# Performance work log

Measured on AMD Instinct MI355X. Metric: run time of the kernel, lower is better.

The kernel has to match this reference:

```python
import jax, jax.numpy as jnp
import numpy as np

K = 16  # num neighbors


def setup_inputs() -> dict:
    key = jax.random.key(0)
    ks = jax.random.split(key, 10)
    B, N, d_in, d_out = 4, 8192, 64, 128
    h = d_out // 2
    return {
        "xyz": jax.random.normal(ks[0], (B, 3, N), jnp.float32),
        "feature": jax.random.normal(ks[1], (B, d_in, N), jnp.float32),
        "w1": jax.random.normal(ks[2], (h, 10), jnp.float32) * 0.1,
        "b1": jax.random.normal(ks[3], (h,), jnp.float32) * 0.1,
        "w2": jax.random.normal(ks[4], (h, h), jnp.float32) * 0.1,
        "b2": jax.random.normal(ks[5], (h,), jnp.float32) * 0.1,
        "w3": jax.random.normal(ks[6], (h, h), jnp.float32) * 0.1,
        "b3": jax.random.normal(ks[7], (h,), jnp.float32) * 0.1,
        "ws": jax.random.normal(ks[8], (d_out, d_in), jnp.float32) * 0.1,
        "bs": jax.random.normal(ks[9], (d_out,), jnp.float32) * 0.1,
    }


def reference(xyz, feature, w1, b1, w2, b2, w3, b3, ws, bs):
    # xyz: [B,3,N], feature: [B,d_in,N]
    xyz_t = jnp.transpose(xyz, (0, 2, 1))  # [B,N,3]
    sq = jnp.sum(xyz_t * xyz_t, axis=-1)  # [B,N]
    # squared pairwise distance [B,N,N]
    dist = sq[:, :, None] + sq[:, None, :] - 2.0 * jnp.einsum("bnc,bmc->bnm", xyz_t, xyz_t)
    _, idx = jax.lax.top_k(-dist, K)  # smallest-k -> [B,N,K]
    # gather neighbor coords: [B,N,K,3]
    knn_xyz = jax.vmap(lambda pts, ind: pts[ind])(xyz_t, idx)
    center = jnp.broadcast_to(xyz_t[:, :, None, :], knn_xyz.shape)  # [B,N,K,3]
    diff = knn_xyz - center
    dsq = jnp.sum(diff * diff, axis=-1, keepdims=True)  # [B,N,K,1]
    pos = jnp.concatenate([center, knn_xyz, diff, dsq], axis=-1)  # [B,N,K,10]
    # three 1x1 convs over channel dim (no activations, faithful to source)
    h = jnp.einsum("bnkc,oc->bnko", pos, w1) + b1
    h = jnp.einsum("bnkc,oc->bnko", h, w2) + b2
    h = jnp.einsum("bnkc,oc->bnko", h, w3) + b3
    fe = jnp.max(h, axis=2)  # max-pool over neighbors -> [B,N,d_out//2]
    fe = jnp.transpose(fe, (0, 2, 1))  # [B,d_out//2,N]
    shortcut = jnp.einsum("bcn,oc->bon", feature, ws) + bs[None, :, None]
    return jnp.concatenate([fe, fe], axis=1) + shortcut  # [B,d_out,N]
```

## Files before the change

### kernel.cpp

```cpp
#include <hip/hip_runtime.h>

#define B_ 4
#define N_ 8192
#define DIN 64
#define HDIM 64
#define DOUT 128
#define KNN 16
#define QPB 64
#define PART 8
#define NTHR (QPB * PART)
#define CHUNK (N_ / PART)
#define CAP 16
#define BLOCKS_PER_B (N_ / QPB)

__global__ __launch_bounds__(256) void k_prep(
    const float* __restrict__ xyz,
    const float* __restrict__ w1, const float* __restrict__ b1,
    const float* __restrict__ w2, const float* __restrict__ b2,
    const float* __restrict__ w3, const float* __restrict__ b3,
    float4* __restrict__ pk, float4* __restrict__ prm) {
  const int blk = blockIdx.x, t = threadIdx.x;
  const int b = blk >> 5;
  const int m = ((blk & 31) << 8) + t;
  const float* xb = xyz + (size_t)b * 3 * N_;
  float x = xb[m], y = xb[N_ + m], z = xb[2 * N_ + m];
  float sq = __fadd_rn(__fadd_rn(__fmul_rn(x, x), __fmul_rn(y, y)), __fmul_rn(z, z));
  pk[((size_t)b << 13) + m] = make_float4(x, y, z, sq);

  if (blk == 0) {
    __shared__ float M2[HDIM][10];
    __shared__ float bb[HDIM];
    const int o = t;
    if (o < HDIM) {
      float r[10];
#pragma unroll
      for (int c = 0; c < 10; c++) r[c] = 0.f;
      float s = b2[o];
      for (int l = 0; l < HDIM; l++) {
        float w = w2[o * HDIM + l];
#pragma unroll
        for (int c = 0; c < 10; c++) r[c] = fmaf(w, w1[l * 10 + c], r[c]);
        s = fmaf(w, b1[l], s);
      }
#pragma unroll
      for (int c = 0; c < 10; c++) M2[o][c] = r[c];
      bb[o] = s;
    }
    __syncthreads();
    if (o < HDIM) {
      float r3[10];
#pragma unroll
      for (int c = 0; c < 10; c++) r3[c] = 0.f;
      float bc = b3[o];
      for (int l = 0; l < HDIM; l++) {
        float w = w3[o * HDIM + l];
#pragma unroll
        for (int c = 0; c < 10; c++) r3[c] = fmaf(w, M2[l][c], r3[c]);
        bc = fmaf(w, bb[l], bc);
      }
      prm[o]      = make_float4(r3[0] - r3[6], r3[1] - r3[7], r3[2] - r3[8], bc);
      prm[64 + o] = make_float4(r3[3] + r3[6], r3[4] + r3[7], r3[5] + r3[8], r3[9]);
    }
  }
}

#define INSERT16(VARR, IARR, VMAX, DVAL, MIDX)                    \
  {                                                               \
    bool done = false;                                            \
    _Pragma("unroll") for (int _i = 0; _i < KNN; _i++) {          \
      bool hit = (!done) && (VARR[_i] == VMAX);                   \
      if (hit) { VARR[_i] = (DVAL); IARR[_i] = (MIDX); }          \
      done = done | hit;                                          \
    }                                                             \
    float _a = fmaxf(fmaxf(fmaxf(VARR[0], VARR[1]), fmaxf(VARR[2], VARR[3])),   \
                     fmaxf(fmaxf(VARR[4], VARR[5]), fmaxf(VARR[6], VARR[7])));  \
    float _b = fmaxf(fmaxf(fmaxf(VARR[8], VARR[9]), fmaxf(VARR[10], VARR[11])), \
                     fmaxf(fmaxf(VARR[12], VARR[13]), fmaxf(VARR[14], VARR[15])));\
    VMAX = fmaxf(_a, _b);                                         \
  }

#define MAX16(VARR, VMAX)                                         \
  {                                                               \
    float _a = fmaxf(fmaxf(fmaxf(VARR[0], VARR[1]), fmaxf(VARR[2], VARR[3])),   \
                     fmaxf(fmaxf(VARR[4], VARR[5]), fmaxf(VARR[6], VARR[7])));  \
    float _b = fmaxf(fmaxf(fmaxf(VARR[8], VARR[9]), fmaxf(VARR[10], VARR[11])), \
                     fmaxf(fmaxf(VARR[12], VARR[13]), fmaxf(VARR[14], VARR[15])));\
    VMAX = fmaxf(_a, _b);                                         \
  }

#define FLUSH()                                                   \
  {                                                               \
    for (int c_ = 0; c_ < cnt; c_++) {                            \
      float fd_ = poolF[c_ * NTHR + t];                           \
      int fm_ = poolI[c_ * NTHR + t];                             \
      if (fd_ < vmax) { INSERT16(v, id, vmax, fd_, fm_); }        \
    }                                                             \
    cnt = 0;                                                      \
    atomicMin(&tau[q], __float_as_uint(vmax));                    \
    gate = fminf(vmax, __uint_as_float(tau[q]));                  \
  }

__global__ __launch_bounds__(NTHR, 4) void k_knn_fe(
    const float4* __restrict__ pk, const float4* __restrict__ prm,
    const float* __restrict__ feature, const float* __restrict__ wsM,
    const float* __restrict__ bs, float* __restrict__ out) {
  const int blk = blockIdx.x;
  const int b  = blk / BLOCKS_PER_B;
  const int n0 = (blk % BLOCKS_PER_B) * QPB;
  const int t = threadIdx.x;
  const int q = t & 63;
  const int j = __builtin_amdgcn_readfirstlane(t >> 6);

  __shared__ unsigned tau[QPB];
  __shared__ float4 prmL[2 * HDIM];
  __shared__ alignas(16) float poolF[CAP * NTHR];
  __shared__ alignas(16) unsigned short poolI[CAP * NTHR];

  if (t < QPB) tau[t] = 0x7f800000u;
  for (int i = t; i < 2 * HDIM; i += NTHR) prmL[i] = prm[i];

  const float4 qv = pk[((size_t)b << 13) + n0 + q];
  const float qx = qv.x, qy = qv.y, qz = qv.z, qs = qv.w;

  const float INF = __uint_as_float(0x7f800000u);
  float v[KNN]; int id[KNN];
  float vmax, gate;
  int cnt = 0;
  __syncthreads();

  const float4* pj = pk + ((size_t)b << 13) + j * CHUNK;

  {
    float4 c[KNN];
#pragma unroll
    for (int e = 0; e < KNN; e++) c[e] = pj[e];
#pragma unroll
    for (int e = 0; e < KNN; e++) {
      float dot = fmaf(c[e].z, qz, fmaf(c[e].y, qy, __fmul_rn(c[e].x, qx)));
      v[e] = __fsub_rn(__fadd_rn(qs, c[e].w), __fmul_rn(2.0f, dot));
      id[e] = j * CHUNK + e;
    }
    MAX16(v, vmax);
    atomicMin(&tau[q], __float_as_uint(vmax));
    gate = fminf(vmax, __uint_as_float(tau[q]));
  }

  for (int u0 = KNN; u0 < CHUNK; u0 += 8) {
    if (__any(cnt > CAP - 8)) { FLUSH(); }
    gate = fminf(gate, __uint_as_float(tau[q]));
    float4 c[8];
#pragma unroll
    for (int e = 0; e < 8; e++) c[e] = pj[u0 + e];
#pragma unroll
    for (int e = 0; e < 8; e++) {
      float dot = fmaf(c[e].z, qz, fmaf(c[e].y, qy, __fmul_rn(c[e].x, qx)));
      float d = __fsub_rn(__fadd_rn(qs, c[e].w), __fmul_rn(2.0f, dot));
      if (d < gate) {
        poolF[cnt * NTHR + t] = d;
        poolI[cnt * NTHR + t] = (unsigned short)(j * CHUNK + u0 + e);
        cnt++;
      }
    }
  }
  FLUSH();
  __syncthreads();

#pragma unroll
  for (int i = 0; i < KNN; i++) {
    poolF[(j * KNN + i) * QPB + q] = v[i];
    poolI[(j * KNN + i) * QPB + q] = (unsigned short)id[i];
  }
  __syncthreads();

  float fv[KNN]; int fid[KNN]; float fm = INF;
  if (j < 4) {
    const int l0 = (2 * j) * KNN, r1 = (2 * j + 1) * KNN;
#pragma unroll
    for (int i = 0; i < KNN; i++) {
      fv[i] = poolF[(l0 + i) * QPB + q];
      fid[i] = poolI[(l0 + i) * QPB + q];
    }
    MAX16(fv, fm);
    for (int s = 0; s < KNN; s++) {
      float d = poolF[(r1 + s) * QPB + q];
      if (d < fm) { int m_ = poolI[(r1 + s) * QPB + q]; INSERT16(fv, fid, fm, d, m_); }
    }
#pragma unroll
    for (int i = 0; i < KNN; i++) {
      poolF[(l0 + i) * QPB + q] = fv[i];
      poolI[(l0 + i) * QPB + q] = (unsigned short)fid[i];
    }
  }
  __syncthreads();
  if (j < 2) {
    const int l0 = (4 * j) * KNN, r1 = (4 * j + 2) * KNN;
#pragma unroll
    for (int i = 0; i < KNN; i++) {
      fv[i] = poolF[(l0 + i) * QPB + q];
      fid[i] = poolI[(l0 + i) * QPB + q];
    }
    MAX16(fv, fm);
    for (int s = 0; s < KNN; s++) {
      float d = poolF[(r1 + s) * QPB + q];
      if (d < fm) { int m_ = poolI[(r1 + s) * QPB + q]; INSERT16(fv, fid, fm, d, m_); }
    }
#pragma unroll
    for (int i = 0; i < KNN; i++) {
      poolF[(l0 + i) * QPB + q] = fv[i];
      poolI[(l0 + i) * QPB + q] = (unsigned short)fid[i];
    }
  }
  __syncthreads();
  if (j == 0) {
#pragma unroll
    for (int i = 0; i < KNN; i++) {
      fv[i] = poolF[i * QPB + q];
      fid[i] = poolI[i * QPB + q];
    }
    MAX16(fv, fm);
    for (int s = 0; s < KNN; s++) {
      float d = poolF[(4 * KNN + s) * QPB + q];
      if (d < fm) { int m_ = poolI[(4 * KNN + s) * QPB + q]; INSERT16(fv, fid, fm, d, m_); }
    }
#pragma unroll
    for (int i = 0; i < KNN; i++) poolI[i * QPB + q] = (unsigned short)fid[i];
  }
  __syncthreads();

#pragma unroll
  for (int kk = 0; kk < 2; kk++) {
    int k = j * 2 + kk;
    int m = poolI[k * QPB + q];
    float4 c = pk[((size_t)b << 13) + m];
    float dx = __fsub_rn(c.x, qx), dy = __fsub_rn(c.y, qy), dz = __fsub_rn(c.z, qz);
    float dsq = __fadd_rn(__fadd_rn(__fmul_rn(dx, dx), __fmul_rn(dy, dy)),
                          __fmul_rn(dz, dz));
    poolF[k * QPB + q] = c.x;
    poolF[(KNN + k) * QPB + q] = c.y;
    poolF[(2 * KNN + k) * QPB + q] = c.z;
    poolF[(3 * KNN + k) * QPB + q] = dsq;
  }
  __syncthreads();

  float fo[8];
  {
    float nx[KNN], ny[KNN], nz[KNN], nd[KNN];
#pragma unroll
    for (int k = 0; k < KNN; k++) {
      nx[k] = poolF[k * QPB + q];
      ny[k] = poolF[(KNN + k) * QPB + q];
      nz[k] = poolF[(2 * KNN + k) * QPB + q];
      nd[k] = poolF[(3 * KNN + k) * QPB + q];
    }
#pragma unroll
    for (int oi = 0; oi < 8; oi++) {
      int o = j * 8 + oi;
      float4 pA = prmL[o], pB = prmL[HDIM + o];
      float basev = fmaf(qz, pA.z, fmaf(qy, pA.y, fmaf(qx, pA.x, pA.w)));
      float mx = -INF;
#pragma unroll
      for (int k = 0; k < KNN; k++) {
        float tv = fmaf(nz[k], pB.z,
                   fmaf(ny[k], pB.y,
                   fmaf(nx[k], pB.x, __fmul_rn(nd[k], pB.w))));
        mx = fmaxf(mx, tv);
      }
      fo[oi] = basev + mx;
    }
  }
  __syncthreads();

  float* wsL = poolF;
  float* feL = (float*)poolI;
  for (int i = t; i < DOUT * DIN; i += NTHR) wsL[i] = wsM[i];
#pragma unroll
  for (int r = 0; r < 8; r++) {
    int c = j * 8 + r;
    feL[c * QPB + q] = feature[(size_t)(b * DIN + c) * N_ + n0 + q];
  }
  __syncthreads();

  float acc[16];
#pragma unroll
  for (int oi = 0; oi < 16; oi++) acc[oi] = 0.f;
  for (int c4 = 0; c4 < DIN / 4; c4++) {
    float f0 = feL[(4 * c4 + 0) * QPB + q];
    float f1 = feL[(4 * c4 + 1) * QPB + q];
    float f2 = feL[(4 * c4 + 2) * QPB + q];
    float f3 = feL[(4 * c4 + 3) * QPB + q];
#pragma unroll
    for (int oi = 0; oi < 16; oi++) {
      int o = (oi < 8) ? (j * 8 + oi) : (64 + j * 8 + oi - 8);
      float4 w = ((const float4*)(wsL + o * DIN))[c4];
      acc[oi] = fmaf(w.x, f0, acc[oi]);
      acc[oi] = fmaf(w.y, f1, acc[oi]);
      acc[oi] = fmaf(w.z, f2, acc[oi]);
      acc[oi] = fmaf(w.w, f3, acc[oi]);
    }
  }
  float* ob = out + (size_t)b * DOUT * N_ + n0 + q;
#pragma unroll
  for (int oi = 0; oi < 16; oi++) {
    int o = (oi < 8) ? (j * 8 + oi) : (64 + j * 8 + oi - 8);
    ob[(size_t)o * N_] = acc[oi] + bs[o] + fo[oi & 7];
  }
}

extern "C" void kernel_launch(void* const* d_in, const int* in_sizes, int n_in,
                              void* d_out, int out_size, void* d_ws, size_t ws_size,
                              hipStream_t stream) {
  const float* xyz     = (const float*)d_in[0];
  const float* feature = (const float*)d_in[1];
  const float* w1 = (const float*)d_in[2];
  const float* b1 = (const float*)d_in[3];
  const float* w2 = (const float*)d_in[4];
  const float* b2 = (const float*)d_in[5];
  const float* w3 = (const float*)d_in[6];
  const float* b3 = (const float*)d_in[7];
  const float* wsM = (const float*)d_in[8];
  const float* bs  = (const float*)d_in[9];
  float* out = (float*)d_out;

  float4* prm = (float4*)d_ws;
  float4* pkB = (float4*)((char*)d_ws + 8192);

  hipLaunchKernelGGL(k_prep, dim3(128), dim3(256), 0, stream,
                     xyz, w1, b1, w2, b2, w3, b3, pkB, prm);
  hipLaunchKernelGGL(k_knn_fe, dim3(B_ * BLOCKS_PER_B), dim3(NTHR), 0, stream,
                     pkB, prm, feature, wsM, bs, out);
}
```

Before: 286.4 us.

## Replace per-thread KNN insertion with wave-cooperative radix top-k selection in one fused kernel

```diff
diff --git a/kernel.cpp b/kernel.cpp
--- a/kernel.cpp
+++ b/kernel.cpp
@@ -7,237 +7,200 @@
 #define DOUT 128
 #define KNN 16
 #define QPB 64
-#define PART 8
-#define NTHR (QPB * PART)
-#define CHUNK (N_ / PART)
-#define CAP 16
+#define NTHR 512
 #define BLOCKS_PER_B (N_ / QPB)
 
-__global__ __launch_bounds__(256) void k_prep(
-    const float* __restrict__ xyz,
+__device__ __forceinline__ int mbcnt64(unsigned long long m) {
+  return __builtin_amdgcn_mbcnt_hi((unsigned)(m >> 32),
+         __builtin_amdgcn_mbcnt_lo((unsigned)m, 0));
+}
+__device__ __forceinline__ unsigned mapkey(float d) {
+  unsigned u = __float_as_uint(d);
+  return (d < 0.0f) ? ~u : (u | 0x80000000u);
+}
+__device__ __forceinline__ float rf(float x) {
+  return __int_as_float(__builtin_amdgcn_readfirstlane(__float_as_int(x)));
+}
+
+__device__ __attribute__((noinline))
+float select16(unsigned* skQ, unsigned short* siQ, int cnt, unsigned short* fout) {
+  const int l = threadIdx.x & 63;
+  unsigned k = 0xFFFFFFFFu;
+  unsigned mi = 0xFFFFu;
+  if (l < cnt) { k = skQ[l]; mi = siQ[l]; }
+  unsigned p = 0; int r = KNN;
+  for (int bit = 31; bit >= 0; bit--) {
+    unsigned long long ml = __ballot((int)(((k ^ p) >> bit) == 0u));
+    int c0 = __popcll(ml);
+    if (r > c0) { p |= (1u << bit); r -= c0; }
+  }
+  bool isLT = (k < p), isTie = (k == p);
+  int tieC = __popcll(__ballot((int)isTie));
+  bool keepT = isTie;
+  if (tieC != r) {
+    unsigned mk = isTie ? mi : 0xFFFFFFFFu;
+    unsigned p2 = 0; int r2 = r;
+    for (int bit = 15; bit >= 0; bit--) {
+      unsigned long long ml = __ballot((int)(((mk ^ p2) >> bit) == 0u));
+      int c0 = __popcll(ml);
+      if (r2 > c0) { p2 |= (1u << bit); r2 -= c0; }
+    }
+    keepT = isTie && (mi <= p2);
+  }
+  bool keep = isLT || keepT;
+  unsigned long long km = __ballot((int)keep);
+  int rank = mbcnt64(km);
+  if (fout) {
+    if (keep) fout[rank * QPB] = (unsigned short)mi;
+  } else {
+    if (keep) { skQ[rank] = k; siQ[rank] = (unsigned short)mi; }
+  }
+  unsigned fb = (p & 0x80000000u) ? (p & 0x7FFFFFFFu) : ~p;
+  return __uint_as_float(fb);
+}
+
+__global__ __launch_bounds__(NTHR, 6) void k_lfa(
+    const float* __restrict__ xyz, const float* __restrict__ feature,
     const float* __restrict__ w1, const float* __restrict__ b1,
     const float* __restrict__ w2, const float* __restrict__ b2,
     const float* __restrict__ w3, const float* __restrict__ b3,
-    float4* __restrict__ pk, float4* __restrict__ prm) {
-  const int blk = blockIdx.x, t = threadIdx.x;
-  const int b = blk >> 5;
-  const int m = ((blk & 31) << 8) + t;
-  const float* xb = xyz + (size_t)b * 3 * N_;
-  float x = xb[m], y = xb[N_ + m], z = xb[2 * N_ + m];
-  float sq = __fadd_rn(__fadd_rn(__fmul_rn(x, x), __fmul_rn(y, y)), __fmul_rn(z, z));
-  pk[((size_t)b << 13) + m] = make_float4(x, y, z, sq);
-
-  if (blk == 0) {
-    __shared__ float M2[HDIM][10];
-    __shared__ float bb[HDIM];
-    const int o = t;
-    if (o < HDIM) {
-      float r[10];
-#pragma unroll
-      for (int c = 0; c < 10; c++) r[c] = 0.f;
-      float s = b2[o];
-      for (int l = 0; l < HDIM; l++) {
-        float w = w2[o * HDIM + l];
-#pragma unroll
-        for (int c = 0; c < 10; c++) r[c] = fmaf(w, w1[l * 10 + c], r[c]);
-        s = fmaf(w, b1[l], s);
-      }
-#pragma unroll
-      for (int c = 0; c < 10; c++) M2[o][c] = r[c];
-      bb[o] = s;
-    }
-    __syncthreads();
-    if (o < HDIM) {
-      float r3[10];
-#pragma unroll
-      for (int c = 0; c < 10; c++) r3[c] = 0.f;
-      float bc = b3[o];
-      for (int l = 0; l < HDIM; l++) {
-        float w = w3[o * HDIM + l];
-#pragma unroll
-        for (int c = 0; c < 10; c++) r3[c] = fmaf(w, M2[l][c], r3[c]);
-        bc = fmaf(w, bb[l], bc);
-      }
-      prm[o]      = make_float4(r3[0] - r3[6], r3[1] - r3[7], r3[2] - r3[8], bc);
-      prm[64 + o] = make_float4(r3[3] + r3[6], r3[4] + r3[7], r3[5] + r3[8], r3[9]);
-    }
-  }
-}
-
-#define INSERT16(VARR, IARR, VMAX, DVAL, MIDX)                    \
-  {                                                               \
-    bool done = false;                                            \
-    _Pragma("unroll") for (int _i = 0; _i < KNN; _i++) {          \
-      bool hit = (!done) && (VARR[_i] == VMAX);                   \
-      if (hit) { VARR[_i] = (DVAL); IARR[_i] = (MIDX); }          \
-      done = done | hit;                                          \
-    }                                                             \
-    float _a = fmaxf(fmaxf(fmaxf(VARR[0], VARR[1]), fmaxf(VARR[2], VARR[3])),   \
-                     fmaxf(fmaxf(VARR[4], VARR[5]), fmaxf(VARR[6], VARR[7])));  \
-    float _b = fmaxf(fmaxf(fmaxf(VARR[8], VARR[9]), fmaxf(VARR[10], VARR[11])), \
-                     fmaxf(fmaxf(VARR[12], VARR[13]), fmaxf(VARR[14], VARR[15])));\
-    VMAX = fmaxf(_a, _b);                                         \
-  }
-
-#define MAX16(VARR, VMAX)                                         \
-  {                                                               \
-    float _a = fmaxf(fmaxf(fmaxf(VARR[0], VARR[1]), fmaxf(VARR[2], VARR[3])),   \
-                     fmaxf(fmaxf(VARR[4], VARR[5]), fmaxf(VARR[6], VARR[7])));  \
-    float _b = fmaxf(fmaxf(fmaxf(VARR[8], VARR[9]), fmaxf(VARR[10], VARR[11])), \
-                     fmaxf(fmaxf(VARR[12], VARR[13]), fmaxf(VARR[14], VARR[15])));\
-    VMAX = fmaxf(_a, _b);                                         \
-  }
-
-#define FLUSH()                                                   \
-  {                                                               \
-    for (int c_ = 0; c_ < cnt; c_++) {                            \
-      float fd_ = poolF[c_ * NTHR + t];                           \
-      int fm_ = poolI[c_ * NTHR + t];                             \
-      if (fd_ < vmax) { INSERT16(v, id, vmax, fd_, fm_); }        \
-    }                                                             \
-    cnt = 0;                                                      \
-    atomicMin(&tau[q], __float_as_uint(vmax));                    \
-    gate = fminf(vmax, __uint_as_float(tau[q]));                  \
-  }
-
-__global__ __launch_bounds__(NTHR, 4) void k_knn_fe(
-    const float4* __restrict__ pk, const float4* __restrict__ prm,
-    const float* __restrict__ feature, const float* __restrict__ wsM,
-    const float* __restrict__ bs, float* __restrict__ out) {
+    const float* __restrict__ wsM, const float* __restrict__ bs,
+    float* __restrict__ out) {
   const int blk = blockIdx.x;
   const int b  = blk / BLOCKS_PER_B;
   const int n0 = (blk % BLOCKS_PER_B) * QPB;
   const int t = threadIdx.x;
-  const int q = t & 63;
+  const int lane = t & 63;
   const int j = __builtin_amdgcn_readfirstlane(t >> 6);
-
-  __shared__ unsigned tau[QPB];
-  __shared__ float4 prmL[2 * HDIM];
-  __shared__ alignas(16) float poolF[CAP * NTHR];
-  __shared__ alignas(16) unsigned short poolI[CAP * NTHR];
-
-  if (t < QPB) tau[t] = 0x7f800000u;
-  for (int i = t; i < 2 * HDIM; i += NTHR) prmL[i] = prm[i];
-
-  const float4 qv = pk[((size_t)b << 13) + n0 + q];
-  const float qx = qv.x, qy = qv.y, qz = qv.z, qs = qv.w;
-
+  const float* xb = xyz + (size_t)b * 3 * N_;
   const float INF = __uint_as_float(0x7f800000u);
-  float v[KNN]; int id[KNN];
-  float vmax, gate;
-  int cnt = 0;
-  __syncthreads();
-
-  const float4* pj = pk + ((size_t)b << 13) + j * CHUNK;
+
+  __shared__ alignas(16) unsigned char poolRaw[49152];
+  unsigned* skey = (unsigned*)poolRaw;
+  unsigned short* sidx = (unsigned short*)(poolRaw + 16384);
+  unsigned short* fidx = (unsigned short*)(poolRaw + 24576);
+  float4* prmL = (float4*)(poolRaw + 26624);
 
   {
-    float4 c[KNN];
-#pragma unroll
-    for (int e = 0; e < KNN; e++) c[e] = pj[e];
-#pragma unroll
-    for (int e = 0; e < KNN; e++) {
-      float dot = fmaf(c[e].z, qz, fmaf(c[e].y, qy, __fmul_rn(c[e].x, qx)));
-      v[e] = __fsub_rn(__fadd_rn(qs, c[e].w), __fmul_rn(2.0f, dot));
-      id[e] = j * CHUNK + e;
-    }
-    MAX16(v, vmax);
-    atomicMin(&tau[q], __float_as_uint(vmax));
-    gate = fminf(vmax, __uint_as_float(tau[q]));
-  }
-
-  for (int u0 = KNN; u0 < CHUNK; u0 += 8) {
-    if (__any(cnt > CAP - 8)) { FLUSH(); }
-    gate = fminf(gate, __uint_as_float(tau[q]));
-    float4 c[8];
-#pragma unroll
-    for (int e = 0; e < 8; e++) c[e] = pj[u0 + e];
-#pragma unroll
-    for (int e = 0; e < 8; e++) {
-      float dot = fmaf(c[e].z, qz, fmaf(c[e].y, qy, __fmul_rn(c[e].x, qx)));
-      float d = __fsub_rn(__fadd_rn(qs, c[e].w), __fmul_rn(2.0f, dot));
-      if (d < gate) {
-        poolF[cnt * NTHR + t] = d;
-        poolI[cnt * NTHR + t] = (unsigned short)(j * CHUNK + u0 + e);
-        cnt++;
-      }
-    }
-  }
-  FLUSH();
-  __syncthreads();
-
-#pragma unroll
-  for (int i = 0; i < KNN; i++) {
-    poolF[(j * KNN + i) * QPB + q] = v[i];
-    poolI[(j * KNN + i) * QPB + q] = (unsigned short)id[i];
-  }
-  __syncthreads();
-
-  float fv[KNN]; int fid[KNN]; float fm = INF;
-  if (j < 4) {
-    const int l0 = (2 * j) * KNN, r1 = (2 * j + 1) * KNN;
-#pragma unroll
-    for (int i = 0; i < KNN; i++) {
-      fv[i] = poolF[(l0 + i) * QPB + q];
-      fid[i] = poolI[(l0 + i) * QPB + q];
-    }
-    MAX16(fv, fm);
-    for (int s = 0; s < KNN; s++) {
-      float d = poolF[(r1 + s) * QPB + q];
-      if (d < fm) { int m_ = poolI[(r1 + s) * QPB + q]; INSERT16(fv, fid, fm, d, m_); }
-    }
-#pragma unroll
-    for (int i = 0; i < KNN; i++) {
-      poolF[(l0 + i) * QPB + q] = fv[i];
-      poolI[(l0 + i) * QPB + q] = (unsigned short)fid[i];
-    }
-  }
-  __syncthreads();
-  if (j < 2) {
-    const int l0 = (4 * j) * KNN, r1 = (4 * j + 2) * KNN;
-#pragma unroll
-    for (int i = 0; i < KNN; i++) {
-      fv[i] = poolF[(l0 + i) * QPB + q];
-      fid[i] = poolI[(l0 + i) * QPB + q];
-    }
-    MAX16(fv, fm);
-    for (int s = 0; s < KNN; s++) {
-      float d = poolF[(r1 + s) * QPB + q];
-      if (d < fm) { int m_ = poolI[(r1 + s) * QPB + q]; INSERT16(fv, fid, fm, d, m_); }
-    }
-#pragma unroll
-    for (int i = 0; i < KNN; i++) {
-      poolF[(l0 + i) * QPB + q] = fv[i];
-      poolI[(l0 + i) * QPB + q] = (unsigned short)fid[i];
-    }
-  }
-  __syncthreads();
-  if (j == 0) {
-#pragma unroll
-    for (int i = 0; i < KNN; i++) {
-      fv[i] = poolF[i * QPB + q];
-      fid[i] = poolI[i * QPB + q];
-    }
-    MAX16(fv, fm);
-    for (int s = 0; s < KNN; s++) {
-      float d = poolF[(4 * KNN + s) * QPB + q];
-      if (d < fm) { int m_ = poolI[(4 * KNN + s) * QPB + q]; INSERT16(fv, fid, fm, d, m_); }
-    }
-#pragma unroll
-    for (int i = 0; i < KNN; i++) poolI[i * QPB + q] = (unsigned short)fid[i];
-  }
-  __syncthreads();
-
+    float* M2 = (float*)poolRaw;
+    float* bbv = (float*)(poolRaw + 2560);
+    if (t < HDIM) {
+      float r[10];
+#pragma unroll
+      for (int c = 0; c < 10; c++) r[c] = 0.f;
+      float s = b2[t];
+      for (int ll = 0; ll < HDIM; ll++) {
+        float w = w2[t * HDIM + ll];
+#pragma unroll
+        for (int c = 0; c < 10; c++) r[c] = fmaf(w, w1[ll * 10 + c], r[c]);
+        s = fmaf(w, b1[ll], s);
+      }
+#pragma unroll
+      for (int c = 0; c < 10; c++) M2[t * 10 + c] = r[c];
+      bbv[t] = s;
+    }
+    __syncthreads();
+    if (t < HDIM) {
+      float r3[10];
+#pragma unroll
+      for (int c = 0; c < 10; c++) r3[c] = 0.f;
+      float bc = b3[t];
+      for (int ll = 0; ll < HDIM; ll++) {
+        float w = w3[t * HDIM + ll];
+#pragma unroll
+        for (int c = 0; c < 10; c++) r3[c] = fmaf(w, M2[ll * 10 + c], r3[c]);
+        bc = fmaf(w, bbv[ll], bc);
+      }
+      prmL[t]      = make_float4(r3[0] - r3[6], r3[1] - r3[7], r3[2] - r3[8], bc);
+      prmL[64 + t] = make_float4(r3[3] + r3[6], r3[4] + r3[7], r3[5] + r3[8], r3[9]);
+    }
+    __syncthreads();
+  }
+
+  float qX[8], qY[8], qZ[8], qS[8];
+#pragma unroll
+  for (int i = 0; i < 8; i++) {
+    int mq = n0 + j * 8 + i;
+    float x = xb[mq], y = xb[N_ + mq], z = xb[2 * N_ + mq];
+    float sq = __fadd_rn(__fadd_rn(__fmul_rn(x, x), __fmul_rn(y, y)), __fmul_rn(z, z));
+    qX[i] = rf(x); qY[i] = rf(y); qZ[i] = rf(z); qS[i] = rf(sq);
+  }
+  float tauF[8]; int cntA[8];
+#pragma unroll
+  for (int i = 0; i < 8; i++) { tauF[i] = INF; cntA[i] = 0; }
+
+  float cx = xb[lane], cy = xb[N_ + lane], cz = xb[2 * N_ + lane];
+  for (int m0 = 0; m0 < N_; m0 += 64) {
+    int mn = (m0 + 64) & (N_ - 1);
+    float px = xb[mn + lane], py = xb[N_ + mn + lane], pz = xb[2 * N_ + mn + lane];
+    float cw = __fadd_rn(__fadd_rn(__fmul_rn(cx, cx), __fmul_rn(cy, cy)),
+                         __fmul_rn(cz, cz));
+    float dd[8];
+#pragma unroll
+    for (int i = 0; i < 8; i++) {
+      float dot = fmaf(cz, qZ[i], fmaf(cy, qY[i], __fmul_rn(cx, qX[i])));
+      dd[i] = __fsub_rn(__fadd_rn(qS[i], cw), __fmul_rn(2.0f, dot));
+    }
+#pragma unroll
+    for (int i = 0; i < 8; i++) {
+      unsigned long long hit = __ballot((int)(dd[i] < tauF[i]));
+      if (hit) {
+        unsigned* skQ = skey + (j * 8 + i) * QPB;
+        unsigned short* siQ = sidx + (j * 8 + i) * QPB;
+        bool mine = dd[i] < tauF[i];
+        int h = __popcll(hit);
+        int rk = mbcnt64(hit);
+        unsigned key = mapkey(dd[i]);
+        unsigned short mm = (unsigned short)(m0 + lane);
+        if (cntA[i] + h <= QPB) {
+          if (mine) { skQ[cntA[i] + rk] = key; siQ[cntA[i] + rk] = mm; }
+          cntA[i] += h;
+          if (cntA[i] == QPB) {
+            tauF[i] = rf(select16(skQ, siQ, QPB, nullptr));
+            cntA[i] = KNN;
+          }
+        } else {
+          unsigned long long rem = hit; bool mrem = mine;
+          while (rem) {
+            int freeS = QPB - cntA[i];
+            int hh = __popcll(rem);
+            int rr = mbcnt64(rem);
+            bool wn = mrem && (rr < freeS);
+            if (wn) { skQ[cntA[i] + rr] = key; siQ[cntA[i] + rr] = mm; }
+            cntA[i] += (hh < freeS) ? hh : freeS;
+            if (cntA[i] == QPB) {
+              tauF[i] = rf(select16(skQ, siQ, QPB, nullptr));
+              cntA[i] = KNN;
+            }
+            mrem = mrem && !wn && (dd[i] < tauF[i]);
+            rem = __ballot((int)mrem);
+          }
+        }
+      }
+    }
+    cx = px; cy = py; cz = pz;
+  }
+#pragma unroll
+  for (int i = 0; i < 8; i++) {
+    select16(skey + (j * 8 + i) * QPB, sidx + (j * 8 + i) * QPB,
+             cntA[i], fidx + (j * 8 + i));
+  }
+  __syncthreads();
+
+  const int q = lane;
+  float qx = xb[n0 + q], qy = xb[N_ + n0 + q], qz = xb[2 * N_ + n0 + q];
+  float* poolF = (float*)poolRaw;
 #pragma unroll
   for (int kk = 0; kk < 2; kk++) {
     int k = j * 2 + kk;
-    int m = poolI[k * QPB + q];
-    float4 c = pk[((size_t)b << 13) + m];
-    float dx = __fsub_rn(c.x, qx), dy = __fsub_rn(c.y, qy), dz = __fsub_rn(c.z, qz);
+    int m = fidx[k * QPB + q];
+    float x = xb[m], y = xb[N_ + m], z = xb[2 * N_ + m];
+    float dx = __fsub_rn(x, qx), dy = __fsub_rn(y, qy), dz = __fsub_rn(z, qz);
     float dsq = __fadd_rn(__fadd_rn(__fmul_rn(dx, dx), __fmul_rn(dy, dy)),
                           __fmul_rn(dz, dz));
-    poolF[k * QPB + q] = c.x;
-    poolF[(KNN + k) * QPB + q] = c.y;
-    poolF[(2 * KNN + k) * QPB + q] = c.z;
+    poolF[k * QPB + q] = x;
+    poolF[(KNN + k) * QPB + q] = y;
+    poolF[(2 * KNN + k) * QPB + q] = z;
     poolF[(3 * KNN + k) * QPB + q] = dsq;
   }
   __syncthreads();
@@ -270,9 +233,9 @@
   }
   __syncthreads();
 
-  float* wsL = poolF;
-  float* feL = (float*)poolI;
-  for (int i = t; i < DOUT * DIN; i += NTHR) wsL[i] = wsM[i];
+  float* wsL = (float*)poolRaw;
+  float* feL = (float*)(poolRaw + 32768);
+  for (int i2 = t; i2 < DOUT * DIN; i2 += NTHR) wsL[i2] = wsM[i2];
 #pragma unroll
   for (int r = 0; r < 8; r++) {
     int c = j * 8 + r;
@@ -321,11 +284,6 @@
   const float* bs  = (const float*)d_in[9];
   float* out = (float*)d_out;
 
-  float4* prm = (float4*)d_ws;
-  float4* pkB = (float4*)((char*)d_ws + 8192);
-
-  hipLaunchKernelGGL(k_prep, dim3(128), dim3(256), 0, stream,
-                     xyz, w1, b1, w2, b2, w3, b3, pkB, prm);
-  hipLaunchKernelGGL(k_knn_fe, dim3(B_ * BLOCKS_PER_B), dim3(NTHR), 0, stream,
-                     pkB, prm, feature, wsM, bs, out);
-}
+  hipLaunchKernelGGL(k_lfa, dim3(B_ * BLOCKS_PER_B), dim3(NTHR), 0, stream,
+                     xyz, feature, w1, b1, w2, b2, w3, b3, wsM, bs, out);
+}
```

After: 427.9 us. 49.4% more time.
